# Kernel tuning notes

Hardware: AMD Instinct MI355X
Metric: run time of the kernel (lower is better)

Reference implementation:

```python
import jax, jax.numpy as jnp
import numpy as np

G = 64  # voxel grid extent per axis; grid_ind entries are in [0, G)


def setup_inputs() -> dict:
    key = jax.random.key(0)
    k1, k2 = jax.random.split(key)
    N = 4_000_000
    points = jax.random.normal(k1, (N, 7), dtype=jnp.float32)
    grid_ind = jax.random.randint(k2, (N, 3), 0, G, dtype=jnp.int64)
    return {"points": points, "grid_ind": grid_ind}


def reference(points, grid_ind):
    # torch.unique(grid_ind, dim=0, return_inverse=True) sorts rows
    # lexicographically; for nonnegative coords that equals sorting the
    # linearized index, so we dedup the linear id instead of rows.
    N = points.shape[0]
    gi = grid_ind.astype(jnp.int32)
    lin = (gi[:, 0] * G + gi[:, 1]) * G + gi[:, 2]  # [N]
    # fixed-size unique for jit compatibility: at most N unique voxels,
    # padded with fill_value=-1 at the tail.
    unq, unq_inv = jnp.unique(lin, return_inverse=True, size=N, fill_value=-1)
    # scatter_mean over point->voxel mapping
    sums = jax.ops.segment_sum(points, unq_inv, num_segments=N)          # [N, 7]
    cnt = jax.ops.segment_sum(jnp.ones((N,), points.dtype), unq_inv,
                              num_segments=N)                            # [N]
    mean = sums / jnp.maximum(cnt, 1.0)[:, None]
    # reconstruct the [n_unique_padded, 3] voxel coordinates (pad rows = -1)
    valid = unq >= 0
    u = jnp.maximum(unq, 0)
    unq3 = jnp.stack([u // (G * G), (u // G) % G, u % G], axis=-1)
    unq3 = jnp.where(valid[:, None], unq3, -1).astype(grid_ind.dtype)
    return mean, unq3
```

## Files before the change

kernel.cpp:

```cpp
#include <hip/hip_runtime.h>

#define NVOX 262144
#define NB   256
#define VPB  1024
#define PPB  2048
#define SCT  512
#define CHK  4096
#define NBLK 256

__global__ void dv_fill(const unsigned* __restrict__ nuP,
                        float* __restrict__ out, int n) {
    int nu = (int)*nuP;
    size_t meanChunks = (size_t)n * 7 / 4;
    size_t coordChunks = (size_t)n * 3 / 4;
    size_t total = meanChunks + coordChunks;
    size_t i = (size_t)blockIdx.x * blockDim.x + threadIdx.x;
    if (i >= total) return;
    float* mean = out;
    float* coords = out + (size_t)n * 7;
    if (i < meanChunks) {
        size_t base = i * 4, lim = (size_t)nu * 7;
        if (base >= lim) {
            *(float4*)(mean + base) = make_float4(0.f, 0.f, 0.f, 0.f);
        } else if (base + 4 > lim) {
            for (size_t k = lim; k < base + 4; ++k) mean[k] = 0.f;
        }
    } else {
        size_t base = (i - meanChunks) * 4, lim = (size_t)nu * 3;
        if (base >= lim) {
            *(float4*)(coords + base) = make_float4(-1.f, -1.f, -1.f, -1.f);
        } else if (base + 4 > lim) {
            for (size_t k = lim; k < base + 4; ++k) coords[k] = -1.f;
        }
    }
}

__device__ __forceinline__ unsigned bf16rne(float x) {
    unsigned u = __float_as_uint(x);
    u += 0x7fffu + ((u >> 16) & 1u);
    return u >> 16;
}

__global__ void __launch_bounds__(SCT) rx_scatfuse(
        const int* __restrict__ gi, const float* __restrict__ pts, int n,
        unsigned* __restrict__ cursor, int capb, uint4* __restrict__ recs) {
    __shared__ uint4 recS[PPB];
    __shared__ unsigned dstS[PPB];
    __shared__ unsigned hist[NB];
    __shared__ unsigned bStart[NB];
    __shared__ unsigned runS[NB];
    __shared__ unsigned wsumS[8];
    int t = threadIdx.x, b = blockIdx.x;
    int lane = t & 63, wid = t >> 6;
    int base = b * PPB;
    int cnt = n - base;
    if (cnt > PPB) cnt = PPB;
    if (t < NB) hist[t] = 0;
    __syncthreads();

    unsigned keyA[PPB / SCT], rankA[PPB / SCT];
    int p0 = base + t * 4;
    bool full = (p0 + 4 <= n);
    if (full) {
        const int4* g4 = (const int4*)(gi + (size_t)base * 3);
        int4 a = g4[3 * t], c = g4[3 * t + 1], d = g4[3 * t + 2];
        keyA[0] = ((unsigned)((a.x << 2) | (a.y >> 4)) << 10) |
                  (unsigned)(((a.y & 15) << 6) | a.z);
        keyA[1] = ((unsigned)((a.w << 2) | (c.x >> 4)) << 10) |
                  (unsigned)(((c.x & 15) << 6) | c.y);
        keyA[2] = ((unsigned)((c.z << 2) | (c.w >> 4)) << 10) |
                  (unsigned)(((c.w & 15) << 6) | d.x);
        keyA[3] = ((unsigned)((d.y << 2) | (d.z >> 4)) << 10) |
                  (unsigned)(((d.z & 15) << 6) | d.w);
#pragma unroll
        for (int j = 0; j < 4; ++j)
            rankA[j] = atomicAdd(&hist[keyA[j] >> 10], 1u);
    } else {
#pragma unroll
        for (int j = 0; j < 4; ++j) {
            int i = p0 + j;
            if (i < n) {
                int g0 = gi[3 * i], g1 = gi[3 * i + 1], g2 = gi[3 * i + 2];
                keyA[j] = ((unsigned)((g0 << 2) | (g1 >> 4)) << 10) |
                          (unsigned)(((g1 & 15) << 6) | g2);
                rankA[j] = atomicAdd(&hist[keyA[j] >> 10], 1u);
            }
        }
    }
    __syncthreads();
    unsigned mine = (t < NB) ? hist[t] : 0u;
    unsigned x = mine;
#pragma unroll
    for (int d = 1; d < 64; d <<= 1) {
        unsigned y = __shfl_up(x, d, 64);
        if (lane >= d) x += y;
    }
    if (t < NB && lane == 63) wsumS[wid] = x;
    __syncthreads();
    if (t < 64) {
        unsigned w = (lane < 4) ? wsumS[lane] : 0u, xx = w;
#pragma unroll
        for (int d = 1; d < 4; d <<= 1) {
            unsigned y = __shfl_up(xx, d, 64);
            if (lane >= d) xx += y;
        }
        if (lane < 4) wsumS[lane] = xx - w;
    }
    __syncthreads();
    if (t < NB) {
        unsigned incl = x + wsumS[wid];
        bStart[t] = incl - mine;
        runS[t] = (mine > 0) ? atomicAdd(&cursor[t], mine) : 0u;
    }
    __syncthreads();

    if (full) {
        float f[28];
        const float4* p4 = (const float4*)(pts + (size_t)base * 7) +
                           (size_t)t * 7;
#pragma unroll
        for (int q = 0; q < 7; ++q) {
            float4 u = p4[q];
            f[q * 4 + 0] = u.x; f[q * 4 + 1] = u.y;
            f[q * 4 + 2] = u.z; f[q * 4 + 3] = u.w;
        }
#pragma unroll
        for (int j = 0; j < 4; ++j) {
            unsigned key = keyA[j], rank = rankA[j];
            unsigned bk = key >> 10, sub = key & 1023u;
            uint4 r;
            r.x = bf16rne(f[j * 7 + 0]) | (bf16rne(f[j * 7 + 1]) << 16);
            r.y = bf16rne(f[j * 7 + 2]) | (bf16rne(f[j * 7 + 3]) << 16);
            r.z = bf16rne(f[j * 7 + 4]) | (bf16rne(f[j * 7 + 5]) << 16);
            r.w = bf16rne(f[j * 7 + 6]) | (sub << 16);
            unsigned sp = bStart[bk] + rank;
            recS[sp] = r;
            dstS[sp] = (unsigned)bk * (unsigned)capb + runS[bk] + rank;
        }
    } else {
#pragma unroll
        for (int j = 0; j < 4; ++j) {
            int lid = t * 4 + j;
            if (lid < cnt) {
                int i = base + lid;
                const float* p = pts + (size_t)i * 7;
                float f0 = p[0], f1 = p[1], f2 = p[2], f3 = p[3];
                float f4 = p[4], f5 = p[5], f6 = p[6];
                unsigned key = keyA[j], rank = rankA[j];
                unsigned bk = key >> 10, sub = key & 1023u;
                uint4 r;
                r.x = bf16rne(f0) | (bf16rne(f1) << 16);
                r.y = bf16rne(f2) | (bf16rne(f3) << 16);
                r.z = bf16rne(f4) | (bf16rne(f5) << 16);
                r.w = bf16rne(f6) | (sub << 16);
                unsigned sp = bStart[bk] + rank;
                recS[sp] = r;
                dstS[sp] = (unsigned)bk * (unsigned)capb + runS[bk] + rank;
            }
        }
    }
    __syncthreads();
#pragma unroll
    for (int k = 0; k < PPB / SCT; ++k) {
        int j = k * SCT + t;
        if (j < cnt) recs[dstS[j]] = recS[j];
    }
}

__global__ void __launch_bounds__(1024) rx_accum(
        const uint4* __restrict__ recs, const unsigned* __restrict__ cursor,
        int capb, float* __restrict__ accTable,
        unsigned* __restrict__ occCount) {
    __shared__ uint4 sortedR[CHK];
    __shared__ unsigned cnt_[VPB];
    __shared__ unsigned wsum[16];
    int t = threadIdx.x, bk = blockIdx.x;
    int lane = t & 63, wid = t >> 6;
    unsigned len = cursor[bk];
    size_t base = (size_t)bk * (unsigned)capb;
    float a0 = 0.f, a1 = 0.f, a2 = 0.f, a3 = 0.f,
          a4 = 0.f, a5 = 0.f, a6 = 0.f, cf = 0.f;
    for (unsigned cs = 0; cs < len; cs += CHK) {
        bool v[4];
        uint4 r[4];
        unsigned k[4], rk[4];
#pragma unroll
        for (int j = 0; j < 4; ++j) {
            v[j] = (cs + j * 1024 + t) < len;
            k[j] = 0; rk[j] = 0;
            if (v[j]) {
                r[j] = recs[base + cs + j * 1024 + t];
                k[j] = r[j].w >> 16;
            }
        }
        cnt_[t] = 0;
        __syncthreads();
#pragma unroll
        for (int j = 0; j < 4; ++j)
            if (v[j]) rk[j] = atomicAdd(&cnt_[k[j]], 1u);
        __syncthreads();
        unsigned own = cnt_[t];
        unsigned x = own;
#pragma unroll
        for (int d = 1; d < 64; d <<= 1) {
            unsigned y = __shfl_up(x, d, 64);
            if (lane >= d) x += y;
        }
        if (lane == 63) wsum[wid] = x;
        __syncthreads();
        if (t < 64) {
            unsigned w = (lane < 16) ? wsum[lane] : 0u;
            unsigned xx = w;
#pragma unroll
            for (int d = 1; d < 16; d <<= 1) {
                unsigned y = __shfl_up(xx, d, 64);
                if (lane >= d) xx += y;
            }
            if (lane < 16) wsum[lane] = xx - w;
        }
        __syncthreads();
        unsigned excl = x - own + wsum[wid];
        cnt_[t] = excl;
        __syncthreads();
#pragma unroll
        for (int j = 0; j < 4; ++j)
            if (v[j]) sortedR[cnt_[k[j]] + rk[j]] = r[j];
        __syncthreads();
        unsigned st = excl, end = excl + own;
        for (unsigned q = st; q < end; ++q) {
            uint4 rr = sortedR[q];
            a0 += __uint_as_float(rr.x << 16);
            a1 += __uint_as_float(rr.x & 0xffff0000u);
            a2 += __uint_as_float(rr.y << 16);
            a3 += __uint_as_float(rr.y & 0xffff0000u);
            a4 += __uint_as_float(rr.z << 16);
            a5 += __uint_as_float(rr.z & 0xffff0000u);
            a6 += __uint_as_float(rr.w << 16);
            cf += 1.f;
        }
        __syncthreads();
    }
    float4* o = (float4*)(accTable + ((size_t)bk * VPB + t) * 8);
    o[0] = make_float4(a0, a1, a2, a3);
    o[1] = make_float4(a4, a5, a6, cf);
    unsigned long long m = __ballot(cf > 0.f);
    if (lane == 0) wsum[wid] = (unsigned)__popcll(m);
    __syncthreads();
    if (t == 0) {
        unsigned occ = 0;
#pragma unroll
        for (int w = 0; w < 16; ++w) occ += wsum[w];
        occCount[bk] = occ;
    }
}

__global__ void rx_emit(const float* __restrict__ accTable,
                        const unsigned* __restrict__ occCount,
                        unsigned* __restrict__ nuOut,
                        float* __restrict__ out_mean,
                        float* __restrict__ out_coords) {
    int bk = blockIdx.x, t = threadIdx.x;

    __shared__ unsigned smB[NB];
    __shared__ unsigned rankBaseS;
    unsigned mineB = occCount[t];
    smB[t] = mineB;
    __syncthreads();
    for (int off = 1; off < NB; off <<= 1) {
        unsigned v = (t >= off) ? smB[t - off] : 0u;
        __syncthreads();
        smB[t] += v;
        __syncthreads();
    }
    if (t == bk) rankBaseS = smB[t] - mineB;
    if (bk == 0 && t == NB - 1) *nuOut = smB[t];
    __syncthreads();

    float row[4][8];
    int pre[4], mycount = 0;
#pragma unroll
    for (int j = 0; j < 4; ++j) {
        int v = t * 4 + j;
        const float4* a = (const float4*)(accTable + ((size_t)bk * VPB + v) * 8);
        float4 r0 = a[0], r1 = a[1];
        row[j][0] = r0.x; row[j][1] = r0.y; row[j][2] = r0.z; row[j][3] = r0.w;
        row[j][4] = r1.x; row[j][5] = r1.y; row[j][6] = r1.z; row[j][7] = r1.w;
        pre[j] = mycount;
        mycount += (row[j][7] > 0.f) ? 1 : 0;
    }
    __shared__ int sm[256];
    sm[t] = mycount;
    __syncthreads();
    for (int off = 1; off < 256; off <<= 1) {
        int v = (t >= off) ? sm[t - off] : 0;
        __syncthreads();
        sm[t] += v;
        __syncthreads();
    }
    int rank0 = (int)rankBaseS + (sm[t] - mycount);
#pragma unroll
    for (int j = 0; j < 4; ++j) {
        if (row[j][7] > 0.f) {
            int r = rank0 + pre[j];
            int lin = (bk << 10) | (t * 4 + j);
            float inv = 1.0f / row[j][7];
            float* m = out_mean + (size_t)r * 7;
#pragma unroll
            for (int k = 0; k < 7; ++k) m[k] = row[j][k] * inv;
            float* cd = out_coords + (size_t)r * 3;
            cd[0] = (float)(lin >> 12);
            cd[1] = (float)((lin >> 6) & 63);
            cd[2] = (float)(lin & 63);
        }
    }
}

struct Meta {
    unsigned blockSums[NBLK];
    unsigned blockFlagSums[NBLK];
    unsigned blockOffs[NBLK];
    unsigned blockRankOffs[NBLK];
    unsigned nUnique;
};

__global__ void dv_count(const int* __restrict__ gi, int n,
                         unsigned* __restrict__ counts,
                         unsigned short* __restrict__ slots) {
    int i = blockIdx.x * blockDim.x + threadIdx.x;
    if (i >= n) return;
    int lin = (gi[3 * i] << 12) | (gi[3 * i + 1] << 6) | gi[3 * i + 2];
    unsigned s = atomicAdd(&counts[lin], 1u);
    slots[i] = (unsigned short)s;
}

__global__ void dv_bs1(const unsigned* __restrict__ counts,
                       Meta* __restrict__ meta) {
    int b = blockIdx.x, t = threadIdx.x;
    uint4 c = ((const uint4*)(counts + (size_t)b * 1024))[t];
    unsigned cs = c.x + c.y + c.z + c.w;
    unsigned fs = (c.x > 0) + (c.y > 0) + (c.z > 0) + (c.w > 0);
    __shared__ unsigned smC[256], smF[256];
    smC[t] = cs; smF[t] = fs;
    __syncthreads();
    for (int off = 128; off > 0; off >>= 1) {
        if (t < off) { smC[t] += smC[t + off]; smF[t] += smF[t + off]; }
        __syncthreads();
    }
    if (t == 0) { meta->blockSums[b] = smC[0]; meta->blockFlagSums[b] = smF[0]; }
}

__global__ void dv_scan2(unsigned* __restrict__ offsets, int n,
                         Meta* __restrict__ meta) {
    __shared__ unsigned smC[NBLK], smF[NBLK];
    int t = threadIdx.x;
    unsigned c = meta->blockSums[t], f = meta->blockFlagSums[t];
    smC[t] = c; smF[t] = f;
    __syncthreads();
    for (int off = 1; off < NBLK; off <<= 1) {
        unsigned vc = (t >= off) ? smC[t - off] : 0u;
        unsigned vf = (t >= off) ? smF[t - off] : 0u;
        __syncthreads();
        smC[t] += vc; smF[t] += vf;
        __syncthreads();
    }
    meta->blockOffs[t] = smC[t] - c;
    meta->blockRankOffs[t] = smF[t] - f;
    if (t == NBLK - 1) { meta->nUnique = smF[t]; offsets[NVOX] = (unsigned)n; }
}

__global__ void dv_scan3(unsigned* __restrict__ counts,
                         const Meta* __restrict__ meta) {
    int b = blockIdx.x, t = threadIdx.x;
    uint4 c = ((const uint4*)(counts + (size_t)b * 1024))[t];
    unsigned mysum = c.x + c.y + c.z + c.w;
    __shared__ unsigned sm[256];
    sm[t] = mysum;
    __syncthreads();
    for (int off = 1; off < 256; off <<= 1) {
        unsigned v = (t >= off) ? sm[t - off] : 0u;
        __syncthreads();
        sm[t] += v;
        __syncthreads();
    }
    unsigned base = meta->blockOffs[b] + sm[t] - mysum;
    uint4 o;
    o.x = base;
    o.y = base + c.x;
    o.z = o.y + c.y;
    o.w = o.z + c.z;
    ((uint4*)(counts + (size_t)b * 1024))[t] = o;
}

__global__ void dv_scatter2(const int* __restrict__ gi, int n,
                            const unsigned* __restrict__ offsets,
                            const unsigned short* __restrict__ slots,
                            unsigned* __restrict__ perm) {
    int i = blockIdx.x * blockDim.x + threadIdx.x;
    if (i >= n) return;
    int lin = (gi[3 * i] << 12) | (gi[3 * i + 1] << 6) | gi[3 * i + 2];
    perm[offsets[lin] + (unsigned)slots[i]] = (unsigned)i;
}

__global__ void dv_emit2(const float* __restrict__ points,
                         const unsigned* __restrict__ offsets,
                         const unsigned* __restrict__ perm,
                         const Meta* __restrict__ meta,
                         float* __restrict__ out_mean,
                         float* __restrict__ out_coords) {
    int b = blockIdx.x, t = threadIdx.x;
    int base = b * 1024 + t * 4;
    uint4 o4 = ((const uint4*)offsets)[b * 256 + t];
    unsigned o[5];
    o[0] = o4.x; o[1] = o4.y; o[2] = o4.z; o[3] = o4.w;
    o[4] = offsets[base + 4];
    int c[4], pre[4], mycount = 0;
#pragma unroll
    for (int j = 0; j < 4; ++j) {
        c[j] = (int)(o[j + 1] - o[j]);
        pre[j] = mycount;
        mycount += (c[j] > 0) ? 1 : 0;
    }
    __shared__ int sm[256];
    sm[t] = mycount;
    __syncthreads();
    for (int off = 1; off < 256; off <<= 1) {
        int v = (t >= off) ? sm[t - off] : 0;
        __syncthreads();
        sm[t] += v;
        __syncthreads();
    }
    int rank0 = (int)meta->blockRankOffs[b] + (sm[t] - mycount);
#pragma unroll
    for (int j = 0; j < 4; ++j) {
        if (c[j] > 0) {
            float s0 = 0.f, s1 = 0.f, s2 = 0.f, s3 = 0.f,
                  s4 = 0.f, s5 = 0.f, s6 = 0.f;
            for (unsigned k = o[j]; k < o[j + 1]; ++k) {
                unsigned idx = perm[k];
                const float* p = points + (size_t)idx * 7;
                s0 += p[0]; s1 += p[1]; s2 += p[2]; s3 += p[3];
                s4 += p[4]; s5 += p[5]; s6 += p[6];
            }
            int r = rank0 + pre[j];
            int v = base + j;
            float inv = 1.0f / (float)c[j];
            float* m = out_mean + (size_t)r * 7;
            m[0] = s0 * inv; m[1] = s1 * inv; m[2] = s2 * inv;
            m[3] = s3 * inv; m[4] = s4 * inv; m[5] = s5 * inv;
            m[6] = s6 * inv;
            float* cd = out_coords + (size_t)r * 3;
            cd[0] = (float)(v >> 12);
            cd[1] = (float)((v >> 6) & 63);
            cd[2] = (float)(v & 63);
        }
    }
}

extern "C" void kernel_launch(void* const* d_in, const int* in_sizes, int n_in,
                              void* d_out, int out_size, void* d_ws, size_t ws_size,
                              hipStream_t stream) {
    const float* points = (const float*)d_in[0];
    const int*   gi     = (const int*)d_in[1];
    int n = in_sizes[0] / 7;

    float* out_mean   = (float*)d_out;
    float* out_coords = (float*)d_out + (size_t)n * 7;

    int threads = 256;
    int nb1 = (n + PPB - 1) / PPB;

    int capb = n / NB + n / NB / 8 + 1024;
    size_t recsB = (size_t)NB * capb * 16;
    size_t accB  = (size_t)NB * VPB * 8 * sizeof(float);
    size_t need  = recsB + accB + NB * 4  + NB * 4  +
                   4  + 256;

    size_t fillChunks = (size_t)n * 7 / 4 + (size_t)n * 3 / 4;
    int fillBlocks = (int)((fillChunks + threads - 1) / threads);

    if (ws_size >= need) {
        char* w = (char*)d_ws;
        uint4*    recs     = (uint4*)w;                    w += recsB;
        float*    accTable = (float*)w;                    w += accB;
        unsigned* cursor   = (unsigned*)w;                 w += NB * 4;
        unsigned* occCount = (unsigned*)w;                 w += NB * 4;
        unsigned* nuTotal  = (unsigned*)w;

        hipMemsetAsync(cursor, 0, NB * 4, stream);
        rx_scatfuse<<<nb1, SCT, 0, stream>>>(gi, points, n, cursor, capb, recs);
        rx_accum<<<NB, 1024, 0, stream>>>(recs, cursor, capb, accTable,
                                          occCount);
        rx_emit<<<NB, 256, 0, stream>>>(accTable, occCount, nuTotal, out_mean,
                                        out_coords);
        dv_fill<<<fillBlocks, threads, 0, stream>>>(nuTotal,
                                                    (float*)d_out, n);
    } else {
        char* w = (char*)d_ws;
        unsigned*       perm    = (unsigned*)w;
        unsigned short* slots   = (unsigned short*)(w + (size_t)n * 4);
        unsigned*       offsets = (unsigned*)(w + (size_t)n * 4 + (size_t)n * 2);
        Meta*           meta    = (Meta*)((char*)offsets + (size_t)(NVOX + 4) * 4);

        hipMemsetAsync(offsets, 0, (size_t)(NVOX + 4) * 4, stream);

        int blocksN = (n + threads - 1) / threads;
        dv_count<<<blocksN, threads, 0, stream>>>(gi, n, offsets, slots);
        dv_bs1<<<NBLK, 256, 0, stream>>>(offsets, meta);
        dv_scan2<<<1, NBLK, 0, stream>>>(offsets, n, meta);
        dv_scan3<<<NBLK, 256, 0, stream>>>(offsets, meta);
        dv_scatter2<<<blocksN, threads, 0, stream>>>(gi, n, offsets, slots, perm);
        dv_emit2<<<NBLK, 256, 0, stream>>>(points, offsets, perm, meta,
                                           out_mean, out_coords);
        dv_fill<<<fillBlocks, threads, 0, stream>>>(&meta->nUnique,
                                                    (float*)d_out, n);
    }
}
```

Measured before the change: 359.7 us.

## Prefetch next record chunk in accumulate and fuse tail fill into emit kernel

The accumulate kernel now issues global loads for the next 4096-record chunk before the per-voxel summation loop, and drops the trailing barrier, so load latency overlaps compute. The emit kernel moves to 1024 threads with one voxel per thread and uses wave-shuffle scans in place of the shared-memory Hillis-Steele scans. It also absorbs the padding fill that used to be a separate dv_fill launch, removing one kernel launch and its global counter round trip. Dropping the end-of-loop barrier relies on the cnt_ reset barrier for correctness. The fused fill runs with only NB*1024 threads in a grid-stride loop.

After: 365.6 us. Within noise of the previous version (+1.6%).

```diff
diff --git a/kernel.cpp b/kernel.cpp
--- a/kernel.cpp
+++ b/kernel.cpp
@@ -180,24 +180,25 @@
     size_t base = (size_t)bk * (unsigned)capb;
     float a0 = 0.f, a1 = 0.f, a2 = 0.f, a3 = 0.f,
           a4 = 0.f, a5 = 0.f, a6 = 0.f, cf = 0.f;
+
+    bool v[4]; uint4 r[4];
+    bool vn[4]; uint4 rn[4];
+#pragma unroll
+    for (int j = 0; j < 4; ++j) {
+        v[j] = ((unsigned)(j * 1024) + t) < len;
+        if (v[j]) r[j] = recs[base + (unsigned)(j * 1024) + t];
+    }
+
     for (unsigned cs = 0; cs < len; cs += CHK) {
-        bool v[4];
-        uint4 r[4];
+        cnt_[t] = 0;
+        __syncthreads();
         unsigned k[4], rk[4];
 #pragma unroll
-        for (int j = 0; j < 4; ++j) {
-            v[j] = (cs + j * 1024 + t) < len;
-            k[j] = 0; rk[j] = 0;
+        for (int j = 0; j < 4; ++j)
             if (v[j]) {
-                r[j] = recs[base + cs + j * 1024 + t];
                 k[j] = r[j].w >> 16;
-            }
-        }
-        cnt_[t] = 0;
-        __syncthreads();
-#pragma unroll
-        for (int j = 0; j < 4; ++j)
-            if (v[j]) rk[j] = atomicAdd(&cnt_[k[j]], 1u);
+                rk[j] = atomicAdd(&cnt_[k[j]], 1u);
+            }
         __syncthreads();
         unsigned own = cnt_[t];
         unsigned x = own;
@@ -225,6 +226,14 @@
 #pragma unroll
         for (int j = 0; j < 4; ++j)
             if (v[j]) sortedR[cnt_[k[j]] + rk[j]] = r[j];
+        unsigned ns = cs + CHK;
+        if (ns < len) {
+#pragma unroll
+            for (int j = 0; j < 4; ++j) {
+                vn[j] = (ns + (unsigned)(j * 1024) + t) < len;
+                if (vn[j]) rn[j] = recs[base + ns + (unsigned)(j * 1024) + t];
+            }
+        }
         __syncthreads();
         unsigned st = excl, end = excl + own;
         for (unsigned q = st; q < end; ++q) {
@@ -238,7 +247,10 @@
             a6 += __uint_as_float(rr.w << 16);
             cf += 1.f;
         }
-        __syncthreads();
+        if (ns < len) {
+#pragma unroll
+            for (int j = 0; j < 4; ++j) { v[j] = vn[j]; if (vn[j]) r[j] = rn[j]; }
+        }
     }
     float4* o = (float4*)(accTable + ((size_t)bk * VPB + t) * 8);
     o[0] = make_float4(a0, a1, a2, a3);
@@ -254,63 +266,104 @@
     }
 }
 
-__global__ void rx_emit(const float* __restrict__ accTable,
-                        const unsigned* __restrict__ occCount,
-                        unsigned* __restrict__ nuOut,
-                        float* __restrict__ out_mean,
-                        float* __restrict__ out_coords) {
+__global__ void __launch_bounds__(1024) rx_emit(
+        const float* __restrict__ accTable,
+        const unsigned* __restrict__ occCount,
+        float* __restrict__ out_mean, float* __restrict__ out_coords,
+        int n) {
     int bk = blockIdx.x, t = threadIdx.x;
-
-    __shared__ unsigned smB[NB];
-    __shared__ unsigned rankBaseS;
-    unsigned mineB = occCount[t];
-    smB[t] = mineB;
-    __syncthreads();
-    for (int off = 1; off < NB; off <<= 1) {
-        unsigned v = (t >= off) ? smB[t - off] : 0u;
-        __syncthreads();
-        smB[t] += v;
-        __syncthreads();
-    }
-    if (t == bk) rankBaseS = smB[t] - mineB;
-    if (bk == 0 && t == NB - 1) *nuOut = smB[t];
-    __syncthreads();
-
-    float row[4][8];
-    int pre[4], mycount = 0;
-#pragma unroll
-    for (int j = 0; j < 4; ++j) {
-        int v = t * 4 + j;
-        const float4* a = (const float4*)(accTable + ((size_t)bk * VPB + v) * 8);
-        float4 r0 = a[0], r1 = a[1];
-        row[j][0] = r0.x; row[j][1] = r0.y; row[j][2] = r0.z; row[j][3] = r0.w;
-        row[j][4] = r1.x; row[j][5] = r1.y; row[j][6] = r1.z; row[j][7] = r1.w;
-        pre[j] = mycount;
-        mycount += (row[j][7] > 0.f) ? 1 : 0;
-    }
-    __shared__ int sm[256];
-    sm[t] = mycount;
-    __syncthreads();
-    for (int off = 1; off < 256; off <<= 1) {
-        int v = (t >= off) ? sm[t - off] : 0;
-        __syncthreads();
-        sm[t] += v;
-        __syncthreads();
-    }
-    int rank0 = (int)rankBaseS + (sm[t] - mycount);
-#pragma unroll
-    for (int j = 0; j < 4; ++j) {
-        if (row[j][7] > 0.f) {
-            int r = rank0 + pre[j];
-            int lin = (bk << 10) | (t * 4 + j);
-            float inv = 1.0f / row[j][7];
-            float* m = out_mean + (size_t)r * 7;
-#pragma unroll
-            for (int k = 0; k < 7; ++k) m[k] = row[j][k] * inv;
-            float* cd = out_coords + (size_t)r * 3;
-            cd[0] = (float)(lin >> 12);
-            cd[1] = (float)((lin >> 6) & 63);
-            cd[2] = (float)(lin & 63);
+    int lane = t & 63, wid = t >> 6;
+    __shared__ unsigned wsB[4];
+    __shared__ unsigned wsum[16];
+    __shared__ unsigned rankBaseS, nuS;
+
+    unsigned mineB = 0, xB = 0;
+    if (t < NB) {
+        mineB = occCount[t];
+        xB = mineB;
+#pragma unroll
+        for (int d = 1; d < 64; d <<= 1) {
+            unsigned y = __shfl_up(xB, d, 64);
+            if (lane >= d) xB += y;
+        }
+        if (lane == 63) wsB[wid] = xB;
+    }
+    __syncthreads();
+    if (t < 64) {
+        unsigned w = (lane < 4) ? wsB[lane] : 0u, xx = w;
+#pragma unroll
+        for (int d = 1; d < 4; d <<= 1) {
+            unsigned y = __shfl_up(xx, d, 64);
+            if (lane >= d) xx += y;
+        }
+        if (lane < 4) wsB[lane] = xx - w;
+    }
+    __syncthreads();
+    if (t < NB) {
+        unsigned incl = xB + wsB[wid];
+        if (t == bk) rankBaseS = incl - mineB;
+        if (t == NB - 1) nuS = incl;
+    }
+    __syncthreads();
+
+    const float4* a = (const float4*)(accTable + ((size_t)bk * VPB + t) * 8);
+    float4 r0 = a[0], r1 = a[1];
+    unsigned flag = (r1.w > 0.f) ? 1u : 0u;
+    unsigned x = flag;
+#pragma unroll
+    for (int d = 1; d < 64; d <<= 1) {
+        unsigned y = __shfl_up(x, d, 64);
+        if (lane >= d) x += y;
+    }
+    if (lane == 63) wsum[wid] = x;
+    __syncthreads();
+    if (t < 64) {
+        unsigned w = (lane < 16) ? wsum[lane] : 0u, xx = w;
+#pragma unroll
+        for (int d = 1; d < 16; d <<= 1) {
+            unsigned y = __shfl_up(xx, d, 64);
+            if (lane >= d) xx += y;
+        }
+        if (lane < 16) wsum[lane] = xx - w;
+    }
+    __syncthreads();
+    unsigned excl = x - flag + wsum[wid];
+    if (flag) {
+        int r = (int)(rankBaseS + excl);
+        int lin = (bk << 10) | t;
+        float inv = 1.0f / r1.w;
+        float* m = out_mean + (size_t)r * 7;
+        m[0] = r0.x * inv; m[1] = r0.y * inv; m[2] = r0.z * inv;
+        m[3] = r0.w * inv; m[4] = r1.x * inv; m[5] = r1.y * inv;
+        m[6] = r1.z * inv;
+        float* cd = out_coords + (size_t)r * 3;
+        cd[0] = (float)(lin >> 12);
+        cd[1] = (float)((lin >> 6) & 63);
+        cd[2] = (float)(lin & 63);
+    }
+
+    int nu = (int)nuS;
+    size_t meanChunks = (size_t)n * 7 / 4;
+    size_t coordChunks = (size_t)n * 3 / 4;
+    size_t total = meanChunks + coordChunks;
+    size_t stride = (size_t)gridDim.x * blockDim.x;
+    float* mean = out_mean;
+    float* coords = out_mean + (size_t)n * 7;
+    for (size_t i = (size_t)bk * blockDim.x + t; i < total; i += stride) {
+        if (i < meanChunks) {
+            size_t base = i * 4, lim = (size_t)nu * 7;
+            if (base >= lim) {
+                *(float4*)(mean + base) = make_float4(0.f, 0.f, 0.f, 0.f);
+            } else if (base + 4 > lim) {
+                for (size_t k = lim; k < base + 4; ++k) mean[k] = 0.f;
+            }
+        } else {
+            size_t base = (i - meanChunks) * 4, lim = (size_t)nu * 3;
+            if (base >= lim) {
+                *(float4*)(coords + base) = make_float4(-1.f, -1.f, -1.f, -1.f);
+            } else if (base + 4 > lim) {
+                for (size_t k = lim; k < base + 4; ++k) coords[k] = -1.f;
+            }
         }
     }
 }
@@ -483,17 +536,14 @@
         uint4*    recs     = (uint4*)w;                    w += recsB;
         float*    accTable = (float*)w;                    w += accB;
         unsigned* cursor   = (unsigned*)w;                 w += NB * 4;
-        unsigned* occCount = (unsigned*)w;                 w += NB * 4;
-        unsigned* nuTotal  = (unsigned*)w;
+        unsigned* occCount = (unsigned*)w;
 
         hipMemsetAsync(cursor, 0, NB * 4, stream);
         rx_scatfuse<<<nb1, SCT, 0, stream>>>(gi, points, n, cursor, capb, recs);
         rx_accum<<<NB, 1024, 0, stream>>>(recs, cursor, capb, accTable,
                                           occCount);
-        rx_emit<<<NB, 256, 0, stream>>>(accTable, occCount, nuTotal, out_mean,
-                                        out_coords);
-        dv_fill<<<fillBlocks, threads, 0, stream>>>(nuTotal,
-                                                    (float*)d_out, n);
+        rx_emit<<<NB, 1024, 0, stream>>>(accTable, occCount, out_mean,
+                                         out_coords, n);
     } else {
         char* w = (char*)d_ws;
         unsigned*       perm    = (unsigned*)w;
```
